# Performance work log

Measured on AMD Instinct MI355X. Metric: run time of the kernel, lower is better.

The kernel has to match this reference:

```python
import jax, jax.numpy as jnp
import numpy as np

T, H, I, E, TOPK = 1024, 1024, 2048, 8, 2


def setup_inputs() -> dict:
    key = jax.random.key(0)
    k1, k2, k3, k4, k5, k6 = jax.random.split(key, 6)
    hidden_states = jax.random.normal(k1, (T, H), dtype=jnp.float32)
    expert_affinities = jax.random.uniform(k2, (T, E), dtype=jnp.float32)
    expert_index = jax.random.randint(k3, (T, TOPK), 0, E, dtype=jnp.int64)
    # Expert GLU MLP weights: gate/up [E,H,I], down [E,I,H]
    w_gate = jax.random.normal(k4, (E, H, I), dtype=jnp.float32) / np.sqrt(H)
    w_up = jax.random.normal(k5, (E, H, I), dtype=jnp.float32) / np.sqrt(H)
    w_down = jax.random.normal(k6, (E, I, H), dtype=jnp.float32) / np.sqrt(I)
    return {
        "hidden_states": hidden_states,
        "expert_affinities": expert_affinities,
        "expert_index": expert_index,
        "w_gate": w_gate,
        "w_up": w_up,
        "w_down": w_down,
        "seq_len": T,
    }


def reference(hidden_states, expert_affinities, expert_index, w_gate, w_up, w_down, seq_len):
    # Gather top-k affinities and renormalize (normalize_top_k_affinities=True)
    topk_aff = jnp.take_along_axis(expert_affinities, expert_index, axis=1)  # [T,K]
    topk_aff = topk_aff / jnp.sum(topk_aff, axis=1, keepdims=True)
    # Dense combine weights [T,E] (scatter of normalized top-k affinities)
    t_idx = jnp.arange(hidden_states.shape[0])[:, None]
    combine = jnp.zeros((hidden_states.shape[0], w_gate.shape[0]),
                        dtype=hidden_states.dtype).at[t_idx, expert_index].add(topk_aff)
    # GLU expert MLP for all experts (E small, grouped-GEMM form)
    g = jnp.einsum("th,ehi->tei", hidden_states, w_gate)  # [T,E,I]
    u = jnp.einsum("th,ehi->tei", hidden_states, w_up)    # [T,E,I]
    act = jax.nn.silu(g) * u                               # [T,E,I]
    # Down-projection fused with affinity-weighted combine
    out = jnp.einsum("tei,eih,te->th", act, w_down, combine)  # [T,H]
    return out
```

## Files before the change

### kernel.cpp

```cpp
#include <hip/hip_runtime.h>
#include <hip/hip_bf16.h>
#include <math.h>

#define T_ 1024
#define H_ 1024
#define I_ 2048
#define E_ 8
#define NSLOT 2048

#define BM 128
#define BN 64
#define BK 32
#define NCHUNK_CAP 24
#define SPLITK2 2

typedef __attribute__((ext_vector_type(8))) short bf16x8;
typedef __attribute__((ext_vector_type(4))) float f32x4;
typedef __attribute__((ext_vector_type(4))) unsigned uint4v;

#define MFMA_BF16 __builtin_amdgcn_mfma_f32_16x16x32_bf16

__device__ __forceinline__ short f2bf(float f) {
  union { float f; unsigned u; } v; v.f = f;
  unsigned r = v.u + 0x7FFFu + ((v.u >> 16) & 1u);
  return (short)(r >> 16);
}
__device__ __forceinline__ unsigned cvtpk(float lo, float hi) {
  unsigned r;
  asm("v_cvt_pk_bf16_f32 %0, %1, %2" : "=v"(r) : "v"(lo), "v"(hi));
  return r;
}
__device__ __forceinline__ void gll16(const void* g, void* l) {
  __builtin_amdgcn_global_load_lds(
      (const __attribute__((address_space(1))) void*)g,
      (__attribute__((address_space(3))) void*)l, 16, 0, 0);
}

__device__ __forceinline__ void pipe_barrier6() {
  __builtin_amdgcn_sched_barrier(0);
  asm volatile("s_waitcnt vmcnt(6) lgkmcnt(0)" ::: "memory");
  __builtin_amdgcn_s_barrier();
  __builtin_amdgcn_sched_barrier(0);
}
__device__ __forceinline__ void drain_barrier() {
  __builtin_amdgcn_sched_barrier(0);
  asm volatile("s_waitcnt vmcnt(0) lgkmcnt(0)" ::: "memory");
  __builtin_amdgcn_s_barrier();
  __builtin_amdgcn_sched_barrier(0);
}

__device__ __forceinline__ unsigned bswz(int n, int kbyte) {
  return (unsigned)(n * 64 + (kbyte ^ (((n >> 2) & 3) << 4)));
}

__global__ __launch_bounds__(256) void k_prep(const float* __restrict__ hs,
                                              short* __restrict__ hs_bf) {
  int i = (blockIdx.x * 256 + threadIdx.x) * 8;
  float4 v0 = *(const float4*)&hs[i];
  float4 v1 = *(const float4*)&hs[i + 4];
  uint4v p;
  p.x = cvtpk(v0.x, v0.y); p.y = cvtpk(v0.z, v0.w);
  p.z = cvtpk(v1.x, v1.y); p.w = cvtpk(v1.z, v1.w);
  *(uint4v*)&hs_bf[i] = p;
}

__global__ __launch_bounds__(1024) void k_build(
    const float* __restrict__ aff, const int* __restrict__ eidx,
    int* __restrict__ meta, int* __restrict__ slot_tok, float* __restrict__ slot_w) {
  __shared__ int cnt[E_];
  __shared__ int soff[E_ + 1];
  int t = threadIdx.x;
  if (t < E_) cnt[t] = 0;
  __syncthreads();
  int e0 = eidx[t * 2 + 0];
  int e1 = eidx[t * 2 + 1];
  float a0 = aff[t * E_ + e0];
  float a1 = aff[t * E_ + e1];
  float inv = 1.0f / (a0 + a1);
  int r0 = atomicAdd(&cnt[e0], 1);
  int r1 = atomicAdd(&cnt[e1], 1);
  __syncthreads();
  if (t == 0) {
    int s = 0;
    for (int e = 0; e < E_; ++e) { soff[e] = s; s += cnt[e]; }
    soff[E_] = s;
    int nc = 0;
    for (int e = 0; e < E_; ++e)
      for (int c = soff[e]; c < soff[e] + cnt[e]; c += BM)
        meta[16 + nc++] = e | (c << 8);
    meta[9] = nc;
  }
  __syncthreads();
  if (t <= E_) meta[t] = soff[t];
  int s0 = soff[e0] + r0;
  int s1 = soff[e1] + r1;
  slot_tok[s0] = t; slot_w[s0] = a0 * inv;
  slot_tok[s1] = t; slot_w[s1] = a1 * inv;
}

__global__ __launch_bounds__(512, 4) void k_gemm1(
    const short* __restrict__ hs_bf, const float* __restrict__ wg,
    const float* __restrict__ wu, const int* __restrict__ meta,
    const int* __restrict__ slot_tok, short* __restrict__ act) {
  int nch = meta[9];
  int yc = blockIdx.y;
  if (yc >= nch) return;
  int ck = meta[16 + yc];
  int e = ck & 255;
  int row0 = ck >> 8;
  int rows = min(BM, meta[1 + e] - row0);
  int i0 = blockIdx.x * BN;

  __shared__ short sA[4][BM * BK];
  __shared__ short sB[2][2][BN * BK];

  int tid = threadIdx.x;
  int lane = tid & 63;
  int w = tid >> 6;
  int wm = w >> 1, wn = w & 1;
  int lr = lane & 15;
  int lk = (lane >> 4) * 8;

  const float* wgE = wg + (size_t)e * H_ * I_;
  const float* wuE = wu + (size_t)e * H_ * I_;

  int ra = 16 * w + (lane >> 2);
  int tokA = slot_tok[row0 + min(ra, rows - 1)];
  const short* srcA = hs_bf + (size_t)tokA * H_ + (lane & 3) * 8;
  const float* wB = (w < 4) ? wgE : wuE;
  int mat = (w >= 4);
  int up = 4 * (w & 3) + (lane >> 4);
  int n4 = (lane & 15) * 4;
  const float* srcB = wB + (size_t)(2 * up) * I_ + i0 + n4;

  f32x4 accg[2][2], accu[2][2];
#pragma unroll
  for (int mr = 0; mr < 2; ++mr)
#pragma unroll
    for (int nr = 0; nr < 2; ++nr) {
      accg[mr][nr] = (f32x4){0.f, 0.f, 0.f, 0.f};
      accu[mr][nr] = (f32x4){0.f, 0.f, 0.f, 0.f};
    }

  float4 bs[4][2];

#pragma unroll
  for (int p = 0; p < 3; ++p) {
    gll16(srcA + p * BK, &sA[p][w * 512]);
    bs[p][0] = *(const float4*)(srcB + (size_t)(p * BK) * I_);
    bs[p][1] = *(const float4*)(srcB + (size_t)(p * BK + 1) * I_);
  }
  {
    const float* p0 = (const float*)&bs[0][0];
    const float* p1 = (const float*)&bs[0][1];
#pragma unroll
    for (int j = 0; j < 4; ++j)
      *(unsigned*)((char*)&sB[0][mat][0] + bswz(n4 + j, 4 * up)) = cvtpk(p0[j], p1[j]);
  }
  drain_barrier();

  const int NT = H_ / BK;

#define G1_ITER(U, base_) do {                                                 \
    int t_ = (base_) + (U);                                                    \
    if (t_ + 3 < NT) {                                                         \
      int k3 = (t_ + 3) * BK;                                                  \
      gll16(srcA + k3, &sA[((U) + 3) & 3][w * 512]);                           \
      bs[((U) + 3) & 3][0] = *(const float4*)(srcB + (size_t)k3 * I_);         \
      bs[((U) + 3) & 3][1] = *(const float4*)(srcB + (size_t)(k3 + 1) * I_);   \
    }                                                                          \
    bf16x8 a0 = *(const bf16x8*)&sA[(U)][(wm * 32 + lr) * BK + lk];            \
    bf16x8 a1 = *(const bf16x8*)&sA[(U)][(wm * 32 + 16 + lr) * BK + lk];       \
    unsigned off0 = bswz(wn * 32 + lr, lk * 2);                                \
    unsigned off1 = bswz(wn * 32 + 16 + lr, lk * 2);                           \
    bf16x8 bg0 = *(const bf16x8*)((const char*)&sB[(U) & 1][0][0] + off0);     \
    bf16x8 bg1 = *(const bf16x8*)((const char*)&sB[(U) & 1][0][0] + off1);     \
    bf16x8 bu0 = *(const bf16x8*)((const char*)&sB[(U) & 1][1][0] + off0);     \
    bf16x8 bu1 = *(const bf16x8*)((const char*)&sB[(U) & 1][1][0] + off1);     \
    accg[0][0] = MFMA_BF16(a0, bg0, accg[0][0], 0, 0, 0);                      \
    accg[0][1] = MFMA_BF16(a0, bg1, accg[0][1], 0, 0, 0);                      \
    accg[1][0] = MFMA_BF16(a1, bg0, accg[1][0], 0, 0, 0);                      \
    accg[1][1] = MFMA_BF16(a1, bg1, accg[1][1], 0, 0, 0);                      \
    accu[0][0] = MFMA_BF16(a0, bu0, accu[0][0], 0, 0, 0);                      \
    accu[0][1] = MFMA_BF16(a0, bu1, accu[0][1], 0, 0, 0);                      \
    accu[1][0] = MFMA_BF16(a1, bu0, accu[1][0], 0, 0, 0);                      \
    accu[1][1] = MFMA_BF16(a1, bu1, accu[1][1], 0, 0, 0);                      \
    if (t_ + 1 < NT) {                                                         \
      const float* p0 = (const float*)&bs[((U) + 1) & 3][0];                   \
      const float* p1 = (const float*)&bs[((U) + 1) & 3][1];                   \
      _Pragma("unroll")                                                        \
      for (int j = 0; j < 4; ++j)                                              \
        *(unsigned*)((char*)&sB[((U) + 1) & 1][mat][0] + bswz(n4 + j, 4 * up)) \
            = cvtpk(p0[j], p1[j]);                                             \
    }                                                                          \
    pipe_barrier6();                                                           \
  } while (0)

  for (int base = 0; base < NT; base += 4) {
    G1_ITER(0, base);
    G1_ITER(1, base);
    G1_ITER(2, base);
    G1_ITER(3, base);
  }
#undef G1_ITER

#pragma unroll
  for (int mr = 0; mr < 2; ++mr) {
#pragma unroll
    for (int r = 0; r < 4; ++r) {
      int m = wm * 32 + mr * 16 + (lane >> 4) * 4 + r;
      if (m < rows) {
#pragma unroll
        for (int nr = 0; nr < 2; ++nr) {
          float g = accg[mr][nr][r];
          float u = accu[mr][nr][r];
          float sg = 1.0f / (1.0f + __expf(-g));
          act[(size_t)(row0 + m) * I_ + i0 + wn * 32 + nr * 16 + lr] = f2bf(g * sg * u);
        }
      }
    }
  }
}

__global__ __launch_bounds__(512, 4) void k_gemm2(
    const short* __restrict__ act, const float* __restrict__ wd,
    const int* __restrict__ meta, const int* __restrict__ slot_tok,
    const float* __restrict__ slot_w, float* __restrict__ out) {
  int nch = meta[9];
  int yc = blockIdx.y;
  if (yc >= nch) return;
  int ck = meta[16 + yc];
  int e = ck & 255;
  int row0 = ck >> 8;
  int rows = min(BM, meta[1 + e] - row0);
  int h0 = blockIdx.x * BN;
  int kbase = blockIdx.z * (I_ / SPLITK2);

  __shared__ short sA[4][BM * BK];
  __shared__ short sB[2][BN * BK];

  int tid = threadIdx.x;
  int lane = tid & 63;
  int w = tid >> 6;
  int wm = w >> 1, wn = w & 1;
  int lr = lane & 15;
  int lk = (lane >> 4) * 8;

  const float* wdE = wd + (size_t)e * I_ * H_;

  int ra = min(16 * w + (lane >> 2), rows - 1);
  const short* srcA = act + (size_t)(row0 + ra) * I_ + kbase + (lane & 3) * 8;
  int up = tid >> 5;
  int n2 = (tid & 31) * 2;
  const float* srcB = wdE + (size_t)(kbase + 2 * up) * H_ + h0 + n2;

  f32x4 acc[2][2];
#pragma unroll
  for (int mr = 0; mr < 2; ++mr)
#pragma unroll
    for (int nr = 0; nr < 2; ++nr)
      acc[mr][nr] = (f32x4){0.f, 0.f, 0.f, 0.f};

  float2 bs[4][2];

#pragma unroll
  for (int p = 0; p < 3; ++p) {
    gll16(srcA + p * BK, &sA[p][w * 512]);
    bs[p][0] = *(const float2*)(srcB + (size_t)(p * BK) * H_);
    bs[p][1] = *(const float2*)(srcB + (size_t)(p * BK + 1) * H_);
  }
  *(unsigned*)((char*)&sB[0][0] + bswz(n2, 4 * up))     = cvtpk(bs[0][0].x, bs[0][1].x);
  *(unsigned*)((char*)&sB[0][0] + bswz(n2 + 1, 4 * up)) = cvtpk(bs[0][0].y, bs[0][1].y);
  drain_barrier();

  const int NT = (I_ / SPLITK2) / BK;

#define G2_ITER(U, base_) do {                                                 \
    int t_ = (base_) + (U);                                                    \
    if (t_ + 3 < NT) {                                                         \
      int k3 = (t_ + 3) * BK;                                                  \
      gll16(srcA + k3, &sA[((U) + 3) & 3][w * 512]);                           \
      bs[((U) + 3) & 3][0] = *(const float2*)(srcB + (size_t)k3 * H_);         \
      bs[((U) + 3) & 3][1] = *(const float2*)(srcB + (size_t)(k3 + 1) * H_);   \
    }                                                                          \
    bf16x8 a0 = *(const bf16x8*)&sA[(U)][(wm * 32 + lr) * BK + lk];            \
    bf16x8 a1 = *(const bf16x8*)&sA[(U)][(wm * 32 + 16 + lr) * BK + lk];       \
    bf16x8 b0 = *(const bf16x8*)((const char*)&sB[(U) & 1][0]                  \
                                 + bswz(wn * 32 + lr, lk * 2));                \
    bf16x8 b1 = *(const bf16x8*)((const char*)&sB[(U) & 1][0]                  \
                                 + bswz(wn * 32 + 16 + lr, lk * 2));           \
    acc[0][0] = MFMA_BF16(a0, b0, acc[0][0], 0, 0, 0);                         \
    acc[0][1] = MFMA_BF16(a0, b1, acc[0][1], 0, 0, 0);                         \
    acc[1][0] = MFMA_BF16(a1, b0, acc[1][0], 0, 0, 0);                         \
    acc[1][1] = MFMA_BF16(a1, b1, acc[1][1], 0, 0, 0);                         \
    if (t_ + 1 < NT) {                                                         \
      int s_ = ((U) + 1) & 3;                                                  \
      *(unsigned*)((char*)&sB[((U) + 1) & 1][0] + bswz(n2, 4 * up))            \
          = cvtpk(bs[s_][0].x, bs[s_][1].x);                                   \
      *(unsigned*)((char*)&sB[((U) + 1) & 1][0] + bswz(n2 + 1, 4 * up))        \
          = cvtpk(bs[s_][0].y, bs[s_][1].y);                                   \
    }                                                                          \
    pipe_barrier6();                                                           \
  } while (0)

  for (int base = 0; base < NT; base += 4) {
    G2_ITER(0, base);
    G2_ITER(1, base);
    G2_ITER(2, base);
    G2_ITER(3, base);
  }
#undef G2_ITER

#pragma unroll
  for (int mr = 0; mr < 2; ++mr) {
#pragma unroll
    for (int r = 0; r < 4; ++r) {
      int m = wm * 32 + mr * 16 + (lane >> 4) * 4 + r;
      if (m < rows) {
        int gs = row0 + m;
        float wc = slot_w[gs];
        int tok = slot_tok[gs];
#pragma unroll
        for (int nr = 0; nr < 2; ++nr)
          atomicAdd(&out[(size_t)tok * H_ + h0 + wn * 32 + nr * 16 + lr],
                    acc[mr][nr][r] * wc);
      }
    }
  }
}

extern "C" void kernel_launch(void* const* d_in, const int* in_sizes, int n_in,
                              void* d_out, int out_size, void* d_ws, size_t ws_size,
                              hipStream_t stream) {
  const float* hs   = (const float*)d_in[0];
  const float* aff  = (const float*)d_in[1];
  const int*   eidx = (const int*)d_in[2];
  const float* wg   = (const float*)d_in[3];
  const float* wu   = (const float*)d_in[4];
  const float* wd   = (const float*)d_in[5];
  float* out = (float*)d_out;

  char* ws = (char*)d_ws;
  int*   meta     = (int*)ws;
  int*   slot_tok = (int*)(ws + 256);
  float* slot_w   = (float*)(ws + 256 + NSLOT * 4);
  short* hs_bf    = (short*)(ws + 256 + NSLOT * 8);
  short* act      = (short*)(ws + 256 + NSLOT * 8 + (size_t)T_ * H_ * 2);

  hipMemsetAsync(d_out, 0, (size_t)out_size * sizeof(float), stream);
  k_build<<<1, T_, 0, stream>>>(aff, eidx, meta, slot_tok, slot_w);
  k_prep<<<(T_ * H_) / (256 * 8), 256, 0, stream>>>(hs, hs_bf);
  k_gemm1<<<dim3(I_ / BN, NCHUNK_CAP), 512, 0, stream>>>(hs_bf, wg, wu, meta, slot_tok, act);
  k_gemm2<<<dim3(H_ / BN, NCHUNK_CAP, SPLITK2), 512, 0, stream>>>(act, wd, meta, slot_tok, slot_w, out);
}
```

Measured before the change: 102.2 us.

## Halve block threads, give each warp 64x32 tiles, swizzle A tile in LDS

Result: no change. 103.1 us (+0.9%).

```diff
diff --git a/kernel.cpp b/kernel.cpp
--- a/kernel.cpp
+++ b/kernel.cpp
@@ -9,14 +9,16 @@
 #define NSLOT 2048
 
 #define BM 128
-#define BN 64
 #define BK 32
+#define BN1 64
+#define BN2 64
 #define NCHUNK_CAP 24
 #define SPLITK2 2
 
 typedef __attribute__((ext_vector_type(8))) short bf16x8;
 typedef __attribute__((ext_vector_type(4))) float f32x4;
 typedef __attribute__((ext_vector_type(4))) unsigned uint4v;
+typedef __attribute__((ext_vector_type(2))) unsigned uint2v;
 
 #define MFMA_BF16 __builtin_amdgcn_mfma_f32_16x16x32_bf16
 
@@ -42,6 +44,12 @@
   __builtin_amdgcn_s_barrier();
   __builtin_amdgcn_sched_barrier(0);
 }
+__device__ __forceinline__ void pipe_barrier4() {
+  __builtin_amdgcn_sched_barrier(0);
+  asm volatile("s_waitcnt vmcnt(4) lgkmcnt(0)" ::: "memory");
+  __builtin_amdgcn_s_barrier();
+  __builtin_amdgcn_sched_barrier(0);
+}
 __device__ __forceinline__ void drain_barrier() {
   __builtin_amdgcn_sched_barrier(0);
   asm volatile("s_waitcnt vmcnt(0) lgkmcnt(0)" ::: "memory");
@@ -49,8 +57,9 @@
   __builtin_amdgcn_sched_barrier(0);
 }
 
-__device__ __forceinline__ unsigned bswz(int n, int kbyte) {
-  return (unsigned)(n * 64 + (kbyte ^ (((n >> 2) & 3) << 4)));
+__device__ __forceinline__ int rswz(int row) { return (row >> 1) & 3; }
+__device__ __forceinline__ unsigned tile_addr(int row, int g) {
+  return (unsigned)(row * 64 + (((g ^ rswz(row)) & 3) << 4));
 }
 
 __global__ __launch_bounds__(256) void k_prep(const float* __restrict__ hs,
@@ -98,232 +107,298 @@
   slot_tok[s1] = t; slot_w[s1] = a1 * inv;
 }
 
-__global__ __launch_bounds__(512, 4) void k_gemm1(
+__global__ __launch_bounds__(256, 2) void k_gemm1(
     const short* __restrict__ hs_bf, const float* __restrict__ wg,
     const float* __restrict__ wu, const int* __restrict__ meta,
     const int* __restrict__ slot_tok, short* __restrict__ act) {
   int nch = meta[9];
-  int yc = blockIdx.y;
-  if (yc >= nch) return;
-  int ck = meta[16 + yc];
+  if (blockIdx.y >= nch) return;
+  int ck = meta[16 + blockIdx.y];
   int e = ck & 255;
   int row0 = ck >> 8;
   int rows = min(BM, meta[1 + e] - row0);
-  int i0 = blockIdx.x * BN;
+  int i0 = blockIdx.x * BN1;
 
   __shared__ short sA[4][BM * BK];
-  __shared__ short sB[2][2][BN * BK];
+  __shared__ short sB[2][2][BN1 * BK];
 
   int tid = threadIdx.x;
   int lane = tid & 63;
   int w = tid >> 6;
   int wm = w >> 1, wn = w & 1;
   int lr = lane & 15;
-  int lk = (lane >> 4) * 8;
+  int g = lane >> 4;
 
   const float* wgE = wg + (size_t)e * H_ * I_;
   const float* wuE = wu + (size_t)e * H_ * I_;
 
-  int ra = 16 * w + (lane >> 2);
-  int tokA = slot_tok[row0 + min(ra, rows - 1)];
-  const short* srcA = hs_bf + (size_t)tokA * H_ + (lane & 3) * 8;
-  const float* wB = (w < 4) ? wgE : wuE;
-  int mat = (w >= 4);
-  int up = 4 * (w & 3) + (lane >> 4);
-  int n4 = (lane & 15) * 4;
-  const float* srcB = wB + (size_t)(2 * up) * I_ + i0 + n4;
-
-  f32x4 accg[2][2], accu[2][2];
-#pragma unroll
-  for (int mr = 0; mr < 2; ++mr)
-#pragma unroll
-    for (int nr = 0; nr < 2; ++nr) {
-      accg[mr][nr] = (f32x4){0.f, 0.f, 0.f, 0.f};
-      accu[mr][nr] = (f32x4){0.f, 0.f, 0.f, 0.f};
+  int r_a0 = 32 * w + (lane >> 2);
+  int r_a1 = r_a0 + 16;
+  int tok0 = slot_tok[row0 + min(r_a0, rows - 1)];
+  int tok1 = slot_tok[row0 + min(r_a1, rows - 1)];
+  const short* srcA0 = hs_bf + (size_t)tok0 * H_ + ((((lane & 3) ^ rswz(r_a0)) & 3) << 3);
+  const short* srcA1 = hs_bf + (size_t)tok1 * H_ + ((((lane & 3) ^ rswz(r_a1)) & 3) << 3);
+
+  int mat = tid >> 7;
+  int kq = (tid >> 4) & 7;
+  int nq = tid & 15;
+  const float* srcB = (mat ? wuE : wgE) + (size_t)(4 * kq) * I_ + i0 + 4 * nq;
+
+  f32x4 accg[4][2], accu[4][2];
+#pragma unroll
+  for (int mf = 0; mf < 4; ++mf)
+#pragma unroll
+    for (int nf = 0; nf < 2; ++nf) {
+      accg[mf][nf] = (f32x4){0.f, 0.f, 0.f, 0.f};
+      accu[mf][nf] = (f32x4){0.f, 0.f, 0.f, 0.f};
     }
 
-  float4 bs[4][2];
-
-#pragma unroll
-  for (int p = 0; p < 3; ++p) {
-    gll16(srcA + p * BK, &sA[p][w * 512]);
-    bs[p][0] = *(const float4*)(srcB + (size_t)(p * BK) * I_);
-    bs[p][1] = *(const float4*)(srcB + (size_t)(p * BK + 1) * I_);
-  }
+  f32x4 bs0[4], bs1[4];
+
+  const int NT = H_ / BK;
+
+  gll16(srcA0, &sA[0][(32 * w) * 32]);
+  gll16(srcA1, &sA[0][(32 * w + 16) * 32]);
+#pragma unroll
+  for (int j = 0; j < 4; ++j) bs0[j] = *(const f32x4*)(srcB + (size_t)j * I_);
+  gll16(srcA0 + BK, &sA[1][(32 * w) * 32]);
+  gll16(srcA1 + BK, &sA[1][(32 * w + 16) * 32]);
+#pragma unroll
+  for (int j = 0; j < 4; ++j) bs1[j] = *(const f32x4*)(srcB + (size_t)(BK + j) * I_);
   {
-    const float* p0 = (const float*)&bs[0][0];
-    const float* p1 = (const float*)&bs[0][1];
-#pragma unroll
-    for (int j = 0; j < 4; ++j)
-      *(unsigned*)((char*)&sB[0][mat][0] + bswz(n4 + j, 4 * up)) = cvtpk(p0[j], p1[j]);
+    char* dst = (char*)&sB[0][mat][0];
+#pragma unroll
+    for (int c = 0; c < 4; ++c) {
+      int n = 4 * nq + c;
+      uint2v wv;
+      wv.x = cvtpk(bs0[0][c], bs0[1][c]);
+      wv.y = cvtpk(bs0[2][c], bs0[3][c]);
+      *(uint2v*)(dst + tile_addr(n, kq >> 1) + ((kq & 1) << 3)) = wv;
+    }
   }
   drain_barrier();
 
-  const int NT = H_ / BK;
-
-#define G1_ITER(U, base_) do {                                                 \
-    int t_ = (base_) + (U);                                                    \
-    if (t_ + 3 < NT) {                                                         \
-      int k3 = (t_ + 3) * BK;                                                  \
-      gll16(srcA + k3, &sA[((U) + 3) & 3][w * 512]);                           \
-      bs[((U) + 3) & 3][0] = *(const float4*)(srcB + (size_t)k3 * I_);         \
-      bs[((U) + 3) & 3][1] = *(const float4*)(srcB + (size_t)(k3 + 1) * I_);   \
+#define G1_ITER(U, bsL, bsC) do {                                              \
+    int t_ = base + (U);                                                       \
+    const char* curA = (const char*)&sA[t_ & 3][0];                            \
+    if (t_ + 2 < NT) {                                                         \
+      short* nxtA = &sA[(t_ + 2) & 3][0];                                      \
+      gll16(srcA0 + (size_t)(t_ + 2) * BK, nxtA + (32 * w) * 32);              \
+      gll16(srcA1 + (size_t)(t_ + 2) * BK, nxtA + (32 * w + 16) * 32);         \
+      const float* sb = srcB + (size_t)(t_ + 2) * BK * I_;                     \
+      bsL[0] = *(const f32x4*)(sb);                                            \
+      bsL[1] = *(const f32x4*)(sb + I_);                                       \
+      bsL[2] = *(const f32x4*)(sb + 2 * I_);                                   \
+      bsL[3] = *(const f32x4*)(sb + 3 * I_);                                   \
     }                                                                          \
-    bf16x8 a0 = *(const bf16x8*)&sA[(U)][(wm * 32 + lr) * BK + lk];            \
-    bf16x8 a1 = *(const bf16x8*)&sA[(U)][(wm * 32 + 16 + lr) * BK + lk];       \
-    unsigned off0 = bswz(wn * 32 + lr, lk * 2);                                \
-    unsigned off1 = bswz(wn * 32 + 16 + lr, lk * 2);                           \
-    bf16x8 bg0 = *(const bf16x8*)((const char*)&sB[(U) & 1][0][0] + off0);     \
-    bf16x8 bg1 = *(const bf16x8*)((const char*)&sB[(U) & 1][0][0] + off1);     \
-    bf16x8 bu0 = *(const bf16x8*)((const char*)&sB[(U) & 1][1][0] + off0);     \
-    bf16x8 bu1 = *(const bf16x8*)((const char*)&sB[(U) & 1][1][0] + off1);     \
-    accg[0][0] = MFMA_BF16(a0, bg0, accg[0][0], 0, 0, 0);                      \
-    accg[0][1] = MFMA_BF16(a0, bg1, accg[0][1], 0, 0, 0);                      \
-    accg[1][0] = MFMA_BF16(a1, bg0, accg[1][0], 0, 0, 0);                      \
-    accg[1][1] = MFMA_BF16(a1, bg1, accg[1][1], 0, 0, 0);                      \
-    accu[0][0] = MFMA_BF16(a0, bu0, accu[0][0], 0, 0, 0);                      \
-    accu[0][1] = MFMA_BF16(a0, bu1, accu[0][1], 0, 0, 0);                      \
-    accu[1][0] = MFMA_BF16(a1, bu0, accu[1][0], 0, 0, 0);                      \
-    accu[1][1] = MFMA_BF16(a1, bu1, accu[1][1], 0, 0, 0);                      \
+    bf16x8 a0 = *(const bf16x8*)(curA + tile_addr(wm * 64 + lr, g));           \
+    bf16x8 a1 = *(const bf16x8*)(curA + tile_addr(wm * 64 + 16 + lr, g));      \
+    bf16x8 a2 = *(const bf16x8*)(curA + tile_addr(wm * 64 + 32 + lr, g));      \
+    bf16x8 a3 = *(const bf16x8*)(curA + tile_addr(wm * 64 + 48 + lr, g));      \
+    const char* pg = (const char*)&sB[(U)][0][0];                              \
+    const char* pu = (const char*)&sB[(U)][1][0];                              \
+    unsigned ob0 = tile_addr(wn * 32 + lr, g);                                 \
+    unsigned ob1 = tile_addr(wn * 32 + 16 + lr, g);                            \
+    bf16x8 g0 = *(const bf16x8*)(pg + ob0);                                    \
+    bf16x8 g1 = *(const bf16x8*)(pg + ob1);                                    \
+    bf16x8 u0 = *(const bf16x8*)(pu + ob0);                                    \
+    bf16x8 u1 = *(const bf16x8*)(pu + ob1);                                    \
+    accg[0][0] = MFMA_BF16(a0, g0, accg[0][0], 0, 0, 0);                       \
+    accg[0][1] = MFMA_BF16(a0, g1, accg[0][1], 0, 0, 0);                       \
+    accg[1][0] = MFMA_BF16(a1, g0, accg[1][0], 0, 0, 0);                       \
+    accg[1][1] = MFMA_BF16(a1, g1, accg[1][1], 0, 0, 0);                       \
+    accg[2][0] = MFMA_BF16(a2, g0, accg[2][0], 0, 0, 0);                       \
+    accg[2][1] = MFMA_BF16(a2, g1, accg[2][1], 0, 0, 0);                       \
+    accg[3][0] = MFMA_BF16(a3, g0, accg[3][0], 0, 0, 0);                       \
+    accg[3][1] = MFMA_BF16(a3, g1, accg[3][1], 0, 0, 0);                       \
+    accu[0][0] = MFMA_BF16(a0, u0, accu[0][0], 0, 0, 0);                       \
+    accu[0][1] = MFMA_BF16(a0, u1, accu[0][1], 0, 0, 0);                       \
+    accu[1][0] = MFMA_BF16(a1, u0, accu[1][0], 0, 0, 0);                       \
+    accu[1][1] = MFMA_BF16(a1, u1, accu[1][1], 0, 0, 0);                       \
+    accu[2][0] = MFMA_BF16(a2, u0, accu[2][0], 0, 0, 0);                       \
+    accu[2][1] = MFMA_BF16(a2, u1, accu[2][1], 0, 0, 0);                       \
+    accu[3][0] = MFMA_BF16(a3, u0, accu[3][0], 0, 0, 0);                       \
+    accu[3][1] = MFMA_BF16(a3, u1, accu[3][1], 0, 0, 0);                       \
     if (t_ + 1 < NT) {                                                         \
-      const float* p0 = (const float*)&bs[((U) + 1) & 3][0];                   \
-      const float* p1 = (const float*)&bs[((U) + 1) & 3][1];                   \
+      char* dst = (char*)&sB[(U) ^ 1][mat][0];                                 \
       _Pragma("unroll")                                                        \
-      for (int j = 0; j < 4; ++j)                                              \
-        *(unsigned*)((char*)&sB[((U) + 1) & 1][mat][0] + bswz(n4 + j, 4 * up)) \
-            = cvtpk(p0[j], p1[j]);                                             \
+      for (int c = 0; c < 4; ++c) {                                            \
+        int n = 4 * nq + c;                                                    \
+        uint2v wv;                                                             \
+        wv.x = cvtpk(bsC[0][c], bsC[1][c]);                                    \
+        wv.y = cvtpk(bsC[2][c], bsC[3][c]);                                    \
+        *(uint2v*)(dst + tile_addr(n, kq >> 1) + ((kq & 1) << 3)) = wv;        \
+      }                                                                        \
     }                                                                          \
     pipe_barrier6();                                                           \
   } while (0)
 
-  for (int base = 0; base < NT; base += 4) {
-    G1_ITER(0, base);
-    G1_ITER(1, base);
-    G1_ITER(2, base);
-    G1_ITER(3, base);
+  for (int base = 0; base < NT; base += 2) {
+    G1_ITER(0, bs0, bs1);
+    G1_ITER(1, bs1, bs0);
   }
 #undef G1_ITER
 
 #pragma unroll
-  for (int mr = 0; mr < 2; ++mr) {
+  for (int mf = 0; mf < 4; ++mf) {
 #pragma unroll
     for (int r = 0; r < 4; ++r) {
-      int m = wm * 32 + mr * 16 + (lane >> 4) * 4 + r;
+      int m = wm * 64 + mf * 16 + g * 4 + r;
       if (m < rows) {
 #pragma unroll
-        for (int nr = 0; nr < 2; ++nr) {
-          float g = accg[mr][nr][r];
-          float u = accu[mr][nr][r];
-          float sg = 1.0f / (1.0f + __expf(-g));
-          act[(size_t)(row0 + m) * I_ + i0 + wn * 32 + nr * 16 + lr] = f2bf(g * sg * u);
+        for (int nf = 0; nf < 2; ++nf) {
+          float gv = accg[mf][nf][r];
+          float uv = accu[mf][nf][r];
+          float sg = 1.0f / (1.0f + __expf(-gv));
+          act[(size_t)(row0 + m) * I_ + i0 + wn * 32 + nf * 16 + lr] = f2bf(gv * sg * uv);
         }
       }
     }
   }
 }
 
-__global__ __launch_bounds__(512, 4) void k_gemm2(
+__global__ __launch_bounds__(256, 2) void k_gemm2(
     const short* __restrict__ act, const float* __restrict__ wd,
     const int* __restrict__ meta, const int* __restrict__ slot_tok,
     const float* __restrict__ slot_w, float* __restrict__ out) {
   int nch = meta[9];
-  int yc = blockIdx.y;
-  if (yc >= nch) return;
-  int ck = meta[16 + yc];
+  if (blockIdx.y >= nch) return;
+  int ck = meta[16 + blockIdx.y];
   int e = ck & 255;
   int row0 = ck >> 8;
   int rows = min(BM, meta[1 + e] - row0);
-  int h0 = blockIdx.x * BN;
+  int h0 = blockIdx.x * BN2;
   int kbase = blockIdx.z * (I_ / SPLITK2);
 
   __shared__ short sA[4][BM * BK];
-  __shared__ short sB[2][BN * BK];
+  __shared__ short sB[2][BN2 * BK];
 
   int tid = threadIdx.x;
   int lane = tid & 63;
   int w = tid >> 6;
   int wm = w >> 1, wn = w & 1;
   int lr = lane & 15;
-  int lk = (lane >> 4) * 8;
+  int g = lane >> 4;
 
   const float* wdE = wd + (size_t)e * I_ * H_;
 
-  int ra = min(16 * w + (lane >> 2), rows - 1);
-  const short* srcA = act + (size_t)(row0 + ra) * I_ + kbase + (lane & 3) * 8;
-  int up = tid >> 5;
-  int n2 = (tid & 31) * 2;
-  const float* srcB = wdE + (size_t)(kbase + 2 * up) * H_ + h0 + n2;
-
-  f32x4 acc[2][2];
-#pragma unroll
-  for (int mr = 0; mr < 2; ++mr)
-#pragma unroll
-    for (int nr = 0; nr < 2; ++nr)
-      acc[mr][nr] = (f32x4){0.f, 0.f, 0.f, 0.f};
-
-  float2 bs[4][2];
-
-#pragma unroll
-  for (int p = 0; p < 3; ++p) {
-    gll16(srcA + p * BK, &sA[p][w * 512]);
-    bs[p][0] = *(const float2*)(srcB + (size_t)(p * BK) * H_);
-    bs[p][1] = *(const float2*)(srcB + (size_t)(p * BK + 1) * H_);
-  }
-  *(unsigned*)((char*)&sB[0][0] + bswz(n2, 4 * up))     = cvtpk(bs[0][0].x, bs[0][1].x);
-  *(unsigned*)((char*)&sB[0][0] + bswz(n2 + 1, 4 * up)) = cvtpk(bs[0][0].y, bs[0][1].y);
+  int isB = (w < 2);
+  int kq = (tid >> 4) & 7;
+  int nq = tid & 15;
+  const float* srcB = wdE + (size_t)(kbase + 4 * kq) * H_ + h0 + 4 * nq;
+  int wp = w & 1;
+  int r_a = 64 * wp + (lane >> 2);
+  const short* srcA[4];
+#pragma unroll
+  for (int p = 0; p < 4; ++p) {
+    int rr = r_a + 16 * p;
+    int gs = ((lane & 3) ^ rswz(rr)) & 3;
+    srcA[p] = act + (size_t)(row0 + min(rr, rows - 1)) * I_ + kbase + (gs << 3);
+  }
+
+  f32x4 acc[4][2];
+#pragma unroll
+  for (int mf = 0; mf < 4; ++mf)
+#pragma unroll
+    for (int nf = 0; nf < 2; ++nf)
+      acc[mf][nf] = (f32x4){0.f, 0.f, 0.f, 0.f};
+
+  f32x4 bs0[4], bs1[4];
+
+  const int NT = (I_ / SPLITK2) / BK;
+
+  if (isB) {
+#pragma unroll
+    for (int j = 0; j < 4; ++j) bs0[j] = *(const f32x4*)(srcB + (size_t)j * H_);
+#pragma unroll
+    for (int j = 0; j < 4; ++j) bs1[j] = *(const f32x4*)(srcB + (size_t)(BK + j) * H_);
+  } else {
+#pragma unroll
+    for (int p = 0; p < 4; ++p)
+      gll16(srcA[p], &sA[0][(64 * wp + 16 * p) * 32]);
+#pragma unroll
+    for (int p = 0; p < 4; ++p)
+      gll16(srcA[p] + BK, &sA[1][(64 * wp + 16 * p) * 32]);
+  }
+  if (isB) {
+    char* dst = (char*)&sB[0][0];
+#pragma unroll
+    for (int c = 0; c < 4; ++c) {
+      int n = 4 * nq + c;
+      uint2v wv;
+      wv.x = cvtpk(bs0[0][c], bs0[1][c]);
+      wv.y = cvtpk(bs0[2][c], bs0[3][c]);
+      *(uint2v*)(dst + tile_addr(n, kq >> 1) + ((kq & 1) << 3)) = wv;
+    }
+  }
   drain_barrier();
 
-  const int NT = (I_ / SPLITK2) / BK;
-
-#define G2_ITER(U, base_) do {                                                 \
-    int t_ = (base_) + (U);                                                    \
-    if (t_ + 3 < NT) {                                                         \
-      int k3 = (t_ + 3) * BK;                                                  \
-      gll16(srcA + k3, &sA[((U) + 3) & 3][w * 512]);                           \
-      bs[((U) + 3) & 3][0] = *(const float2*)(srcB + (size_t)k3 * H_);         \
-      bs[((U) + 3) & 3][1] = *(const float2*)(srcB + (size_t)(k3 + 1) * H_);   \
+#define G2_ITER(U, bsL, bsC) do {                                              \
+    int t_ = base + (U);                                                       \
+    const char* curA = (const char*)&sA[t_ & 3][0];                            \
+    if (t_ + 2 < NT) {                                                         \
+      if (isB) {                                                               \
+        const float* sb = srcB + (size_t)(t_ + 2) * BK * H_;                   \
+        bsL[0] = *(const f32x4*)(sb);                                          \
+        bsL[1] = *(const f32x4*)(sb + H_);                                     \
+        bsL[2] = *(const f32x4*)(sb + 2 * H_);                                 \
+        bsL[3] = *(const f32x4*)(sb + 3 * H_);                                 \
+      } else {                                                                 \
+        short* nxtA = &sA[(t_ + 2) & 3][0];                                    \
+        gll16(srcA[0] + (size_t)(t_ + 2) * BK, nxtA + (64 * wp) * 32);         \
+        gll16(srcA[1] + (size_t)(t_ + 2) * BK, nxtA + (64 * wp + 16) * 32);    \
+        gll16(srcA[2] + (size_t)(t_ + 2) * BK, nxtA + (64 * wp + 32) * 32);    \
+        gll16(srcA[3] + (size_t)(t_ + 2) * BK, nxtA + (64 * wp + 48) * 32);    \
+      }                                                                        \
     }                                                                          \
-    bf16x8 a0 = *(const bf16x8*)&sA[(U)][(wm * 32 + lr) * BK + lk];            \
-    bf16x8 a1 = *(const bf16x8*)&sA[(U)][(wm * 32 + 16 + lr) * BK + lk];       \
-    bf16x8 b0 = *(const bf16x8*)((const char*)&sB[(U) & 1][0]                  \
-                                 + bswz(wn * 32 + lr, lk * 2));                \
-    bf16x8 b1 = *(const bf16x8*)((const char*)&sB[(U) & 1][0]                  \
-                                 + bswz(wn * 32 + 16 + lr, lk * 2));           \
+    bf16x8 a0 = *(const bf16x8*)(curA + tile_addr(wm * 64 + lr, g));           \
+    bf16x8 a1 = *(const bf16x8*)(curA + tile_addr(wm * 64 + 16 + lr, g));      \
+    bf16x8 a2 = *(const bf16x8*)(curA + tile_addr(wm * 64 + 32 + lr, g));      \
+    bf16x8 a3 = *(const bf16x8*)(curA + tile_addr(wm * 64 + 48 + lr, g));      \
+    const char* pb = (const char*)&sB[(U)][0];                                 \
+    bf16x8 b0 = *(const bf16x8*)(pb + tile_addr(wn * 32 + lr, g));             \
+    bf16x8 b1 = *(const bf16x8*)(pb + tile_addr(wn * 32 + 16 + lr, g));        \
     acc[0][0] = MFMA_BF16(a0, b0, acc[0][0], 0, 0, 0);                         \
     acc[0][1] = MFMA_BF16(a0, b1, acc[0][1], 0, 0, 0);                         \
     acc[1][0] = MFMA_BF16(a1, b0, acc[1][0], 0, 0, 0);                         \
     acc[1][1] = MFMA_BF16(a1, b1, acc[1][1], 0, 0, 0);                         \
-    if (t_ + 1 < NT) {                                                         \
-      int s_ = ((U) + 1) & 3;                                                  \
-      *(unsigned*)((char*)&sB[((U) + 1) & 1][0] + bswz(n2, 4 * up))            \
-          = cvtpk(bs[s_][0].x, bs[s_][1].x);                                   \
-      *(unsigned*)((char*)&sB[((U) + 1) & 1][0] + bswz(n2 + 1, 4 * up))        \
-          = cvtpk(bs[s_][0].y, bs[s_][1].y);                                   \
+    acc[2][0] = MFMA_BF16(a2, b0, acc[2][0], 0, 0, 0);                         \
+    acc[2][1] = MFMA_BF16(a2, b1, acc[2][1], 0, 0, 0);                         \
+    acc[3][0] = MFMA_BF16(a3, b0, acc[3][0], 0, 0, 0);                         \
+    acc[3][1] = MFMA_BF16(a3, b1, acc[3][1], 0, 0, 0);                         \
+    if (isB && t_ + 1 < NT) {                                                  \
+      char* dst = (char*)&sB[(U) ^ 1][0];                                      \
+      _Pragma("unroll")                                                        \
+      for (int c = 0; c < 4; ++c) {                                            \
+        int n = 4 * nq + c;                                                    \
+        uint2v wv;                                                             \
+        wv.x = cvtpk(bsC[0][c], bsC[1][c]);                                    \
+        wv.y = cvtpk(bsC[2][c], bsC[3][c]);                                    \
+        *(uint2v*)(dst + tile_addr(n, kq >> 1) + ((kq & 1) << 3)) = wv;        \
+      }                                                                        \
     }                                                                          \
-    pipe_barrier6();                                                           \
+    pipe_barrier4();                                                           \
   } while (0)
 
-  for (int base = 0; base < NT; base += 4) {
-    G2_ITER(0, base);
-    G2_ITER(1, base);
-    G2_ITER(2, base);
-    G2_ITER(3, base);
+  for (int base = 0; base < NT; base += 2) {
+    G2_ITER(0, bs0, bs1);
+    G2_ITER(1, bs1, bs0);
   }
 #undef G2_ITER
 
 #pragma unroll
-  for (int mr = 0; mr < 2; ++mr) {
+  for (int mf = 0; mf < 4; ++mf) {
 #pragma unroll
     for (int r = 0; r < 4; ++r) {
-      int m = wm * 32 + mr * 16 + (lane >> 4) * 4 + r;
+      int m = wm * 64 + mf * 16 + g * 4 + r;
       if (m < rows) {
         int gs = row0 + m;
         float wc = slot_w[gs];
         int tok = slot_tok[gs];
 #pragma unroll
-        for (int nr = 0; nr < 2; ++nr)
-          atomicAdd(&out[(size_t)tok * H_ + h0 + wn * 32 + nr * 16 + lr],
-                    acc[mr][nr][r] * wc);
+        for (int nf = 0; nf < 2; ++nf)
+          atomicAdd(&out[(size_t)tok * H_ + h0 + wn * 32 + nf * 16 + lr],
+                    acc[mf][nf][r] * wc);
       }
     }
   }
@@ -350,6 +425,6 @@
   hipMemsetAsync(d_out, 0, (size_t)out_size * sizeof(float), stream);
   k_build<<<1, T_, 0, stream>>>(aff, eidx, meta, slot_tok, slot_w);
   k_prep<<<(T_ * H_) / (256 * 8), 256, 0, stream>>>(hs, hs_bf);
-  k_gemm1<<<dim3(I_ / BN, NCHUNK_CAP), 512, 0, stream>>>(hs_bf, wg, wu, meta, slot_tok, act);
-  k_gemm2<<<dim3(H_ / BN, NCHUNK_CAP, SPLITK2), 512, 0, stream>>>(act, wd, meta, slot_tok, slot_w, out);
-}
+  k_gemm1<<<dim3(I_ / BN1, NCHUNK_CAP), 256, 0, stream>>>(hs_bf, wg, wu, meta, slot_tok, act);
+  k_gemm2<<<dim3(H_ / BN2, NCHUNK_CAP, SPLITK2), 256, 0, stream>>>(act, wd, meta, slot_tok, slot_w, out);
+}
```
